# Optimization experiments

Hardware: AMD Instinct MI355X
Metric: run time of the kernel (lower is better)

The kernel has to match this reference:

```python
import jax, jax.numpy as jnp
import numpy as np

B, S, D, H, DH = 2, 1024, 1024, 16, 64
SCALE = 1.0 / np.sqrt(DH)


def setup_inputs() -> dict:
    key = jax.random.key(0)
    ks = jax.random.split(key, 9)
    return {
        "x": jax.random.normal(ks[0], (B, S, D), jnp.float32),
        "qkv_w": jax.random.normal(ks[1], (3 * H * DH, D), jnp.float32) * 0.02,
        "out_w": jax.random.normal(ks[2], (D, H * DH), jnp.float32) * 0.02,
        "bias_p": jax.random.uniform(ks[3], (H, 1, 1), jnp.float32) * 2.0,
        "bias_a": jax.random.uniform(ks[4], (H, 1, 1), jnp.float32),
        "mlp_w1": jax.random.normal(ks[5], (H, 2 * H), jnp.float32) * 0.1,
        "mlp_b1": jnp.zeros((H,), jnp.float32),
        "mlp_w2": jax.random.normal(ks[6], (H, H), jnp.float32) * 0.1,
        "mlp_b2": jnp.zeros((H,), jnp.float32),
    }


def reference(x, qkv_w, out_w, bias_p, bias_a, mlp_w1, mlp_b1, mlp_w2, mlp_b2):
    # qkv projection: torch Linear => x @ W.T
    qkv = (x @ qkv_w.T).reshape(B, S, 3, H, DH)
    q = qkv[:, :, 0].transpose(0, 2, 1, 3)  # [B,H,S,DH]
    k = qkv[:, :, 1].transpose(0, 2, 1, 3)
    v = qkv[:, :, 2].transpose(0, 2, 1, 3)

    scores = jnp.einsum('bhqd,bhkd->bhqk', q, k) * SCALE  # [B,H,S,S]

    # Kerple additive bias: -p * log1p(a * |i-j|), per head
    p = jnp.clip(bias_p, 0.01)
    a = jnp.clip(bias_a, 0.01)
    pos = jnp.arange(S, dtype=jnp.float32)
    dist = jnp.abs(pos[None, :] - pos[:, None])  # [S,S]
    kb = -p * jnp.log1p(a * dist)  # [H,S,S]

    # DAPE refinement MLP over per-(i,j) head features
    z = jnp.concatenate(
        [scores, jnp.broadcast_to(kb[None], (B, H, S, S))], axis=1
    ).transpose(0, 2, 3, 1)  # [B,S,S,2H]
    hdn = jax.nn.gelu(z @ mlp_w1.T + mlp_b1, approximate=False)  # [B,S,S,H]
    refine = (hdn @ mlp_w2.T + mlp_b2).transpose(0, 3, 1, 2)  # [B,H,S,S]

    scores = scores + kb[None] + refine
    attn = jax.nn.softmax(scores, axis=-1)  # dropout is identity in eval

    out = jnp.einsum('bhqk,bhkd->bhqd', attn, v)  # [B,H,S,DH]
    out = out.transpose(0, 2, 1, 3).reshape(B, S, H * DH)
    return out @ out_w.T
```

## Files before the change

### kernel.cpp

```cpp
#include <hip/hip_runtime.h>
#include <math.h>

#define Bsz 2
#define Ssz 1024
#define Dsz 1024
#define Hn 16
#define DHsz 64
#define QKV3 3072
#define SCALE 0.125f

typedef __bf16 bf16;
typedef bf16 bf16x8 __attribute__((ext_vector_type(8)));
typedef bf16 bf16x4 __attribute__((ext_vector_type(4)));
typedef float f32x4 __attribute__((ext_vector_type(4)));

#define MFMA(a, b, c) __builtin_amdgcn_mfma_f32_16x16x32_bf16(a, b, c, 0, 0, 0)
#define LDT 72

__global__ void cast_hi(const float* __restrict__ src, bf16* __restrict__ hi, int n) {
  int idx = (blockIdx.x * 256 + threadIdx.x) * 4;
  if (idx >= n) return;
  float4 v = *(const float4*)(src + idx);
  bf16x4 hv = {(bf16)v.x, (bf16)v.y, (bf16)v.z, (bf16)v.w};
  *(bf16x4*)(hi + idx) = hv;
}

__global__ void kb_table(const float* __restrict__ bias_p, const float* __restrict__ bias_a,
                         float* __restrict__ kbtt) {
  int idx = blockIdx.x * 256 + threadIdx.x;
  int d = idx >> 4, h = idx & 15;
  float p = fmaxf(bias_p[h], 0.01f), a = fmaxf(bias_a[h], 0.01f);
  kbtt[idx] = -p * log1pf(a * (float)d);
}

__global__ void tk_table(const float* __restrict__ kbtt, const float* __restrict__ w1,
                         const float* __restrict__ b1, float2* __restrict__ tk) {
  int idx = blockIdx.x * 256 + threadIdx.x;
  int o = idx >> 4, n = idx & 15;
  int d = o - 1024; if (d < 0) d = -d; if (d > 1023) d = 1023;
  float t1 = b1[n];
#pragma unroll
  for (int h = 0; h < 16; ++h) t1 += w1[n * 32 + 16 + h] * kbtt[d * 16 + h];
  tk[idx] = make_float2(t1, kbtt[d * 16 + n]);
}

__global__ void wfrag(const float* __restrict__ w1, const float* __restrict__ w2,
                      bf16* __restrict__ wf) {
  int lane = threadIdx.x;
  int l15 = lane & 15, q8 = (lane >> 4) << 3;
  bf16x8 w1d, w2a;
#pragma unroll
  for (int e = 0; e < 8; ++e) {
    int k = q8 + e;
    if (k < 16) {
      w1d[e] = (bf16)w1[l15 * 32 + k];
    } else {
      float w = w1[l15 * 32 + k - 16];
      w1d[e] = (bf16)(w - (float)(bf16)w);
    }
    w2a[e] = (bf16)w2[l15 * 16 + (k & 15)];
  }
  *(bf16x8*)(wf + lane * 8) = w1d;
  *(bf16x8*)(wf + 512 + lane * 8) = w2a;
}

__global__ __launch_bounds__(256, 3) void k1_qkv(const bf16* __restrict__ A,
                                                 const bf16* __restrict__ B,
                                                 bf16* __restrict__ C) {
  __shared__ __align__(16) bf16 sA[128 * LDT];
  __shared__ __align__(16) bf16 sB[96 * LDT];
  const int tid = threadIdx.x;
  const int lane = tid & 63, wv = tid >> 6;
  const int wr = wv >> 1, wc = wv & 1;
  const int l15 = lane & 15, q8 = (lane >> 4) << 3, q4 = (lane >> 4) << 2;
  const int m0 = blockIdx.y * 128, n0 = blockIdx.x * 96;
  const int r0 = tid >> 3, c8 = (tid & 7) << 3;

  f32x4 acc[4][3];
#pragma unroll
  for (int t = 0; t < 4; ++t)
#pragma unroll
    for (int u = 0; u < 3; ++u)
#pragma unroll
      for (int r = 0; r < 4; ++r) acc[t][u][r] = 0.f;

  bf16x8 rA[4], rB[3];
#define K1_LOAD(kt)                                                         \
  {                                                                         \
    _Pragma("unroll") for (int c = 0; c < 4; ++c)                           \
      rA[c] = *(const bf16x8*)(A + (size_t)(m0 + c * 32 + r0) * Dsz + (kt) + c8);  \
    _Pragma("unroll") for (int c = 0; c < 3; ++c)                           \
      rB[c] = *(const bf16x8*)(B + (size_t)(n0 + c * 32 + r0) * Dsz + (kt) + c8);  \
  }

  K1_LOAD(0)
  for (int kt = 0; kt < Dsz; kt += 64) {
    __syncthreads();
#pragma unroll
    for (int c = 0; c < 4; ++c) *(bf16x8*)&sA[(c * 32 + r0) * LDT + c8] = rA[c];
#pragma unroll
    for (int c = 0; c < 3; ++c) *(bf16x8*)&sB[(c * 32 + r0) * LDT + c8] = rB[c];
    __syncthreads();
    if (kt + 64 < Dsz) K1_LOAD(kt + 64)
#pragma unroll
    for (int ks = 0; ks < 64; ks += 32) {
      bf16x8 fa[4], fb[3];
#pragma unroll
      for (int t = 0; t < 4; ++t)
        fa[t] = *(const bf16x8*)&sA[(wr * 64 + t * 16 + l15) * LDT + ks + q8];
#pragma unroll
      for (int u = 0; u < 3; ++u)
        fb[u] = *(const bf16x8*)&sB[(wc * 48 + u * 16 + l15) * LDT + ks + q8];
#pragma unroll
      for (int t = 0; t < 4; ++t)
#pragma unroll
        for (int u = 0; u < 3; ++u) acc[t][u] = MFMA(fa[t], fb[u], acc[t][u]);
    }
  }
#pragma unroll
  for (int t = 0; t < 4; ++t)
#pragma unroll
    for (int u = 0; u < 3; ++u) {
      int col = n0 + wc * 48 + u * 16 + l15;
#pragma unroll
      for (int r = 0; r < 4; ++r) {
        int row = m0 + wr * 64 + t * 16 + q4 + r;
        C[(size_t)row * QKV3 + col] = (bf16)acc[t][u][r];
      }
    }
#undef K1_LOAD
}

__global__ void pack_vt(const bf16* __restrict__ qkv, bf16* __restrict__ vt) {
  __shared__ __align__(16) bf16 T[64 * LDT];
  const int tid = threadIdx.x;
  const int bh = blockIdx.y, b = bh >> 4, h = bh & 15;
  const int j0 = blockIdx.x * 64;
#pragma unroll
  for (int c = 0; c < 2; ++c) {
    int lin = c * 256 + tid;
    int jr = lin >> 3, d8 = (lin & 7) << 3;
    bf16x8 v = *(const bf16x8*)(qkv + (size_t)(b * Ssz + j0 + jr) * QKV3 + 2048 + h * DHsz + d8);
#pragma unroll
    for (int e = 0; e < 8; ++e) T[(d8 + e) * LDT + jr] = v[e];
  }
  __syncthreads();
#pragma unroll
  for (int c = 0; c < 2; ++c) {
    int lin = c * 256 + tid;
    int d = lin >> 3, j8 = (lin & 7) << 3;
    bf16x8 o = *(const bf16x8*)&T[d * LDT + j8];
    *(bf16x8*)(vt + ((size_t)(b * Hn + h) * DHsz + d) * Ssz + j0 + j8) = o;
  }
}

__global__ __launch_bounds__(256, 3) void k2_qk(const bf16* __restrict__ qkv,
                                                bf16* __restrict__ scores) {
  __shared__ __align__(16) bf16 sA[128 * LDT], sB[128 * LDT];
  const int tid = threadIdx.x;
  const int lane = tid & 63, wv = tid >> 6;
  const int wr = wv >> 1, wc = wv & 1;
  const int l15 = lane & 15, q8 = (lane >> 4) << 3, q4 = (lane >> 4) << 2;
  const int z = blockIdx.z, b = z >> 4, h = z & 15;
  const int i0 = blockIdx.y * 128, j0 = blockIdx.x * 128;
  const bf16* Ab = qkv + (size_t)b * Ssz * QKV3 + h * DHsz;
  const bf16* Bb = Ab + Ssz;
  const int r0 = tid >> 3, c8 = (tid & 7) << 3;
#pragma unroll
  for (int c = 0; c < 4; ++c) {
    int row = c * 32 + r0;
    *(bf16x8*)&sA[row * LDT + c8] = *(const bf16x8*)(Ab + (size_t)(i0 + row) * QKV3 + c8);
    *(bf16x8*)&sB[row * LDT + c8] = *(const bf16x8*)(Bb + (size_t)(j0 + row) * QKV3 + c8);
  }
  __syncthreads();
  f32x4 acc[4][4];
#pragma unroll
  for (int t = 0; t < 4; ++t)
#pragma unroll
    for (int u = 0; u < 4; ++u)
#pragma unroll
      for (int r = 0; r < 4; ++r) acc[t][u][r] = 0.f;
#pragma unroll
  for (int ks = 0; ks < 64; ks += 32) {
    bf16x8 fa[4], fb[4];
#pragma unroll
    for (int t = 0; t < 4; ++t) fa[t] = *(const bf16x8*)&sA[(wr * 64 + t * 16 + l15) * LDT + ks + q8];
#pragma unroll
    for (int u = 0; u < 4; ++u) fb[u] = *(const bf16x8*)&sB[(wc * 64 + u * 16 + l15) * LDT + ks + q8];
#pragma unroll
    for (int t = 0; t < 4; ++t)
#pragma unroll
      for (int u = 0; u < 4; ++u) acc[t][u] = MFMA(fa[t], fb[u], acc[t][u]);
  }
  bf16* dstp = scores + ((size_t)(b * Hn + h) << 20);
#pragma unroll
  for (int t = 0; t < 4; ++t)
#pragma unroll
    for (int u = 0; u < 4; ++u) {
      int col = j0 + wc * 64 + u * 16 + l15;
#pragma unroll
      for (int r = 0; r < 4; ++r) {
        int row = i0 + wr * 64 + t * 16 + q4 + r;
        dstp[((size_t)row << 10) + col] = (bf16)(acc[t][u][r] * SCALE);
      }
    }
}

__device__ __forceinline__ float gelu_fast(float x) {
  float z = fabsf(x) * 0.70710678118654752f;
  float t = __builtin_amdgcn_rcpf(fmaf(0.3275911f, z, 1.0f));
  float poly = t * fmaf(t, fmaf(t, fmaf(t, fmaf(t, 1.061405429f, -1.453152027f),
                                        1.421413741f), -0.284496736f), 0.254829592f);
  float erfa = 1.0f - poly * __expf(-z * z);
  float erfs = copysignf(erfa, x);
  return 0.5f * x * (1.0f + erfs);
}

#define SHS 264
#define LGS 264

__global__ __launch_bounds__(256, 5) void dape_softmax(bf16* scores,
                                                       const float2* __restrict__ tk,
                                                       const bf16* __restrict__ wf,
                                                       const float* __restrict__ b2,
                                                       float* __restrict__ sums) {
  const int c = blockIdx.x;
  const int i = blockIdx.y;
  const int b = blockIdx.z;
  const int tid = threadIdx.x;
  const int lane = tid & 63, wv = tid >> 6;
  const int l15 = lane & 15, q = lane >> 4;
  const int q8 = q << 3, q4 = q << 2;

  __shared__ bf16 sH[Hn][SHS];
  __shared__ float lgt[Hn][LGS];
  __shared__ __align__(16) bf16 hdnS[4][16][40];

  const bf16x8 w1d = *(const bf16x8*)(wf + lane * 8);
  const bf16x8 w2a = *(const bf16x8*)(wf + 512 + lane * 8);
  const float bias2 = b2[l15];

  if (lane < 32) {
    int row = lane >> 1, col = 16 + (lane & 1) * 8;
    *(bf16x8*)&hdnS[wv][row][col] = (bf16x8){};
  }

  const int jw = wv * 64;
  const bf16* srow = scores + ((size_t)(b * Hn) << 20) + ((size_t)i << 10) + c * 256;
#pragma unroll
  for (int t = 0; t < 2; ++t) {
    int h = t * 8 + (lane >> 3);
    int col = jw + (lane & 7) * 8;
    *(bf16x8*)&sH[h][col] = *(const bf16x8*)(srow + ((size_t)h << 20) + col);
  }

  const float2* tkp = tk + ((size_t)(c * 256 + jw + q4 - i + 1024) << 4) + l15;

  for (int jt = 0; jt < 4; ++jt) {
    const int j0c = jw + jt * 16;
    bf16x8 a1;
#pragma unroll
    for (int e = 0; e < 8; ++e) a1[e] = sH[(q8 + e) & 15][j0c + l15];
    float2 tkv[4];
#pragma unroll
    for (int r = 0; r < 4; ++r) tkv[r] = tkp[r * 16];
    f32x4 c1 = {tkv[0].x, tkv[1].x, tkv[2].x, tkv[3].x};
    c1 = MFMA(a1, w1d, c1);
#pragma unroll
    for (int r = 0; r < 4; ++r) hdnS[wv][q4 + r][l15] = (bf16)gelu_fast(c1[r]);
    bf16x8 a2 = *(const bf16x8*)&hdnS[wv][l15][q8];
    f32x4 c2 = {bias2, bias2, bias2, bias2};
    c2 = MFMA(a2, w2a, c2);
    bf16x4 sc4 = *(const bf16x4*)&sH[l15][j0c + q4];
    f32x4 lg;
#pragma unroll
    for (int r = 0; r < 4; ++r) lg[r] = (float)sc4[r] + tkv[r].y + c2[r];
    *(f32x4*)&lgt[l15][j0c + q4] = lg;
    tkp += 256;
  }
  __syncthreads();

#pragma unroll
  for (int hh = 0; hh < 4; ++hh) {
    const int h = wv * 4 + hh;
    f32x4 v0 = *(const f32x4*)&lgt[h][lane * 4];
    float s = 0.f;
#pragma unroll
    for (int e = 0; e < 4; ++e) { v0[e] = __expf(v0[e]); s += v0[e]; }
#pragma unroll
    for (int off = 32; off > 0; off >>= 1) s += __shfl_xor(s, off, 64);
    bf16* dst = scores + ((size_t)(b * Hn + h) << 20) + ((size_t)i << 10) + c * 256;
    bf16x4 p0 = {(bf16)v0[0], (bf16)v0[1], (bf16)v0[2], (bf16)v0[3]};
    *(bf16x4*)(dst + lane * 4) = p0;
    if (lane == 0) sums[((((b << 10) + i) << 4) + h) * 4 + c] = s;
  }
}

__global__ __launch_bounds__(256, 4) void k4_av(const bf16* __restrict__ attn,
                                                const bf16* __restrict__ vt,
                                                const float* __restrict__ sums,
                                                bf16* __restrict__ aout) {
  __shared__ __align__(16) bf16 sA[64 * LDT], sB[64 * LDT];
  const int tid = threadIdx.x;
  const int lane = tid & 63, wv = tid >> 6;
  const int wr = wv >> 1, wc = wv & 1;
  const int l15 = lane & 15, q8 = (lane >> 4) << 3, q4 = (lane >> 4) << 2;
  const int i0 = blockIdx.x * 64, h = blockIdx.y, b = blockIdx.z;
  const bf16* Ab = attn + ((size_t)(b * Hn + h) << 20) + ((size_t)i0 << 10);
  const bf16* Bb = vt + (size_t)(b * Hn + h) * DHsz * Ssz;
  const int r0 = tid >> 3, c8 = (tid & 7) << 3;
  f32x4 acc[2][2];
#pragma unroll
  for (int t = 0; t < 2; ++t)
#pragma unroll
    for (int u = 0; u < 2; ++u)
#pragma unroll
      for (int r = 0; r < 4; ++r) acc[t][u][r] = 0.f;
  bf16x8 rA[2], rB[2];
#define K4_LOAD(kt)                                               \
  {                                                               \
    _Pragma("unroll") for (int c = 0; c < 2; ++c) {               \
      int row = c * 32 + r0;                                      \
      rA[c] = *(const bf16x8*)(Ab + ((size_t)row << 10) + (kt) + c8); \
      rB[c] = *(const bf16x8*)(Bb + ((size_t)row << 10) + (kt) + c8); \
    }                                                             \
  }
  K4_LOAD(0)
  for (int kt = 0; kt < Ssz; kt += 64) {
    __syncthreads();
#pragma unroll
    for (int c = 0; c < 2; ++c) {
      int row = c * 32 + r0;
      *(bf16x8*)&sA[row * LDT + c8] = rA[c];
      *(bf16x8*)&sB[row * LDT + c8] = rB[c];
    }
    __syncthreads();
    if (kt + 64 < Ssz) K4_LOAD(kt + 64)
#pragma unroll
    for (int ks = 0; ks < 64; ks += 32) {
      bf16x8 fa[2], fb[2];
#pragma unroll
      for (int t = 0; t < 2; ++t) fa[t] = *(const bf16x8*)&sA[(wr * 32 + t * 16 + l15) * LDT + ks + q8];
#pragma unroll
      for (int u = 0; u < 2; ++u) fb[u] = *(const bf16x8*)&sB[(wc * 32 + u * 16 + l15) * LDT + ks + q8];
#pragma unroll
      for (int t = 0; t < 2; ++t)
#pragma unroll
        for (int u = 0; u < 2; ++u) acc[t][u] = MFMA(fa[t], fb[u], acc[t][u]);
    }
  }
#pragma unroll
  for (int t = 0; t < 2; ++t)
#pragma unroll
    for (int r = 0; r < 4; ++r) {
      int row = i0 + wr * 32 + t * 16 + q4 + r;
      f32x4 sv = *(const f32x4*)&sums[((((b << 10) + row) << 4) + h) * 4];
      float inv = 1.f / (sv[0] + sv[1] + sv[2] + sv[3]);
#pragma unroll
      for (int u = 0; u < 2; ++u) {
        int d = wc * 32 + u * 16 + l15;
        aout[(size_t)(b * Ssz + row) * Dsz + h * DHsz + d] = (bf16)(acc[t][u][r] * inv);
      }
    }
#undef K4_LOAD
}

__global__ __launch_bounds__(256, 4) void k5_out(const bf16* __restrict__ A,
                                                 const bf16* __restrict__ B,
                                                 float* __restrict__ C) {
  __shared__ __align__(16) bf16 sA[64 * LDT], sB[64 * LDT];
  const int tid = threadIdx.x;
  const int lane = tid & 63, wv = tid >> 6;
  const int wr = wv >> 1, wc = wv & 1;
  const int l15 = lane & 15, q8 = (lane >> 4) << 3, q4 = (lane >> 4) << 2;
  const int m0 = blockIdx.y * 64, n0 = blockIdx.x * 64;
  const int r0 = tid >> 3, c8 = (tid & 7) << 3;
  f32x4 acc[2][2];
#pragma unroll
  for (int t = 0; t < 2; ++t)
#pragma unroll
    for (int u = 0; u < 2; ++u)
#pragma unroll
      for (int r = 0; r < 4; ++r) acc[t][u][r] = 0.f;
  bf16x8 rA[2], rB[2];
#define K5_LOAD(kt)                                                       \
  {                                                                       \
    _Pragma("unroll") for (int c = 0; c < 2; ++c) {                       \
      int row = c * 32 + r0;                                              \
      rA[c] = *(const bf16x8*)(A + (size_t)(m0 + row) * Dsz + (kt) + c8);   \
      rB[c] = *(const bf16x8*)(B + (size_t)(n0 + row) * Dsz + (kt) + c8);   \
    }                                                                     \
  }
  K5_LOAD(0)
  for (int kt = 0; kt < Dsz; kt += 64) {
    __syncthreads();
#pragma unroll
    for (int c = 0; c < 2; ++c) {
      int row = c * 32 + r0;
      *(bf16x8*)&sA[row * LDT + c8] = rA[c];
      *(bf16x8*)&sB[row * LDT + c8] = rB[c];
    }
    __syncthreads();
    if (kt + 64 < Dsz) K5_LOAD(kt + 64)
#pragma unroll
    for (int ks = 0; ks < 64; ks += 32) {
      bf16x8 fa[2], fb[2];
#pragma unroll
      for (int t = 0; t < 2; ++t) fa[t] = *(const bf16x8*)&sA[(wr * 32 + t * 16 + l15) * LDT + ks + q8];
#pragma unroll
      for (int u = 0; u < 2; ++u) fb[u] = *(const bf16x8*)&sB[(wc * 32 + u * 16 + l15) * LDT + ks + q8];
#pragma unroll
      for (int t = 0; t < 2; ++t)
#pragma unroll
        for (int u = 0; u < 2; ++u) acc[t][u] = MFMA(fa[t], fb[u], acc[t][u]);
    }
  }
#pragma unroll
  for (int t = 0; t < 2; ++t)
#pragma unroll
    for (int u = 0; u < 2; ++u) {
      int col = n0 + wc * 32 + u * 16 + l15;
#pragma unroll
      for (int r = 0; r < 4; ++r) {
        int row = m0 + wr * 32 + t * 16 + q4 + r;
        C[(size_t)row * Dsz + col] = acc[t][u][r];
      }
    }
#undef K5_LOAD
}

extern "C" void kernel_launch(void* const* d_in, const int* in_sizes, int n_in,
                              void* d_out, int out_size, void* d_ws, size_t ws_size,
                              hipStream_t stream) {
  const float* x      = (const float*)d_in[0];
  const float* qkv_w  = (const float*)d_in[1];
  const float* out_w  = (const float*)d_in[2];
  const float* bias_p = (const float*)d_in[3];
  const float* bias_a = (const float*)d_in[4];
  const float* w1     = (const float*)d_in[5];
  const float* b1     = (const float*)d_in[6];
  const float* w2     = (const float*)d_in[7];
  const float* b2     = (const float*)d_in[8];
  float* out = (float*)d_out;

  char* ws = (char*)d_ws;
  const size_t MB = 1ull << 20;
  bf16* ow_h   = (bf16*)(ws + 0 * MB);
  bf16* qkv_bf = (bf16*)(ws + 2 * MB);
  bf16* v_t    = (bf16*)(ws + 14 * MB);
  bf16* aout   = (bf16*)(ws + 18 * MB);
  float* kbtt  = (float*)(ws + 22 * MB);
  float* sums  = (float*)(ws + 22 * MB + 65536);
  bf16* wf     = (bf16*)(ws + 22 * MB + 589824);
  float2* tk   = (float2*)(ws + 22 * MB + 655360);
  bf16* x_h    = (bf16*)(ws + 23 * MB);
  bf16* w_h    = (bf16*)(ws + 27 * MB);
  bf16* sc_bf  = (bf16*)(ws + 23 * MB);

  cast_hi<<<2048, 256, 0, stream>>>(x, x_h, Bsz * Ssz * Dsz);
  cast_hi<<<3072, 256, 0, stream>>>(qkv_w, w_h, QKV3 * Dsz);
  cast_hi<<<1024, 256, 0, stream>>>(out_w, ow_h, Dsz * Dsz);
  kb_table<<<64, 256, 0, stream>>>(bias_p, bias_a, kbtt);
  tk_table<<<128, 256, 0, stream>>>(kbtt, w1, b1, tk);
  wfrag<<<1, 64, 0, stream>>>(w1, w2, wf);

  k1_qkv<<<dim3(QKV3 / 96, (Bsz * Ssz) / 128), 256, 0, stream>>>(x_h, w_h, qkv_bf);
  pack_vt<<<dim3(Ssz / 64, Bsz * Hn), 256, 0, stream>>>(qkv_bf, v_t);

  k2_qk<<<dim3(Ssz / 128, Ssz / 128, Bsz * Hn), 256, 0, stream>>>(qkv_bf, sc_bf);
  dape_softmax<<<dim3(4, Ssz, Bsz), 256, 0, stream>>>(sc_bf, tk, wf, b2, sums);
  k4_av<<<dim3(Ssz / 64, Hn, Bsz), 256, 0, stream>>>(sc_bf, v_t, sums, aout);

  k5_out<<<dim3(Dsz / 64, (Bsz * Ssz) / 64), 256, 0, stream>>>(aout, ow_h, out);
}
```

Baseline: 205.7 us.

## Fuse setup kernels and compute softmax exponentials in the DAPE MFMA loop

```diff
diff --git a/kernel.cpp b/kernel.cpp
--- a/kernel.cpp
+++ b/kernel.cpp
@@ -17,51 +17,63 @@
 #define MFMA(a, b, c) __builtin_amdgcn_mfma_f32_16x16x32_bf16(a, b, c, 0, 0, 0)
 #define LDT 72
 
-__global__ void cast_hi(const float* __restrict__ src, bf16* __restrict__ hi, int n) {
+__global__ void cast_all(const float* __restrict__ x, const float* __restrict__ qw,
+                         const float* __restrict__ ow, bf16* __restrict__ xh,
+                         bf16* __restrict__ wh, bf16* __restrict__ owh) {
   int idx = (blockIdx.x * 256 + threadIdx.x) * 4;
-  if (idx >= n) return;
-  float4 v = *(const float4*)(src + idx);
+  const float* src;
+  bf16* dst;
+  int off = idx;
+  if (idx < 2097152) {
+    src = x; dst = xh;
+  } else if (idx < 2097152 + 3145728) {
+    src = qw; dst = wh; off = idx - 2097152;
+  } else {
+    src = ow; dst = owh; off = idx - (2097152 + 3145728);
+  }
+  float4 v = *(const float4*)(src + off);
   bf16x4 hv = {(bf16)v.x, (bf16)v.y, (bf16)v.z, (bf16)v.w};
-  *(bf16x4*)(hi + idx) = hv;
-}
-
-__global__ void kb_table(const float* __restrict__ bias_p, const float* __restrict__ bias_a,
-                         float* __restrict__ kbtt) {
-  int idx = blockIdx.x * 256 + threadIdx.x;
-  int d = idx >> 4, h = idx & 15;
-  float p = fmaxf(bias_p[h], 0.01f), a = fmaxf(bias_a[h], 0.01f);
-  kbtt[idx] = -p * log1pf(a * (float)d);
-}
-
-__global__ void tk_table(const float* __restrict__ kbtt, const float* __restrict__ w1,
-                         const float* __restrict__ b1, float2* __restrict__ tk) {
+  *(bf16x4*)(dst + off) = hv;
+}
+
+__global__ void tk_wfrag(const float* __restrict__ bias_p, const float* __restrict__ bias_a,
+                         const float* __restrict__ w1, const float* __restrict__ b1,
+                         const float* __restrict__ w2, float2* __restrict__ tk,
+                         bf16* __restrict__ wf) {
+  if (blockIdx.x == 128) {
+    int lane = threadIdx.x;
+    if (lane < 64) {
+      int l15 = lane & 15, q8 = (lane >> 4) << 3;
+      bf16x8 w1d, w2a;
+#pragma unroll
+      for (int e = 0; e < 8; ++e) {
+        int k = q8 + e;
+        if (k < 16) {
+          w1d[e] = (bf16)w1[l15 * 32 + k];
+        } else {
+          float w = w1[l15 * 32 + k - 16];
+          w1d[e] = (bf16)(w - (float)(bf16)w);
+        }
+        w2a[e] = (bf16)w2[l15 * 16 + (k & 15)];
+      }
+      *(bf16x8*)(wf + lane * 8) = w1d;
+      *(bf16x8*)(wf + 512 + lane * 8) = w2a;
+    }
+    return;
+  }
   int idx = blockIdx.x * 256 + threadIdx.x;
   int o = idx >> 4, n = idx & 15;
   int d = o - 1024; if (d < 0) d = -d; if (d > 1023) d = 1023;
+  float fd = (float)d;
   float t1 = b1[n];
-#pragma unroll
-  for (int h = 0; h < 16; ++h) t1 += w1[n * 32 + 16 + h] * kbtt[d * 16 + h];
-  tk[idx] = make_float2(t1, kbtt[d * 16 + n]);
-}
-
-__global__ void wfrag(const float* __restrict__ w1, const float* __restrict__ w2,
-                      bf16* __restrict__ wf) {
-  int lane = threadIdx.x;
-  int l15 = lane & 15, q8 = (lane >> 4) << 3;
-  bf16x8 w1d, w2a;
-#pragma unroll
-  for (int e = 0; e < 8; ++e) {
-    int k = q8 + e;
-    if (k < 16) {
-      w1d[e] = (bf16)w1[l15 * 32 + k];
-    } else {
-      float w = w1[l15 * 32 + k - 16];
-      w1d[e] = (bf16)(w - (float)(bf16)w);
-    }
-    w2a[e] = (bf16)w2[l15 * 16 + (k & 15)];
-  }
-  *(bf16x8*)(wf + lane * 8) = w1d;
-  *(bf16x8*)(wf + 512 + lane * 8) = w2a;
+  float t2 = 0.f;
+#pragma unroll
+  for (int h = 0; h < 16; ++h) {
+    float kb = -fmaxf(bias_p[h], 0.01f) * log1pf(fmaxf(bias_a[h], 0.01f) * fd);
+    t1 += w1[n * 32 + 16 + h] * kb;
+    if (h == n) t2 = kb;
+  }
+  tk[idx] = make_float2(t1, t2);
 }
 
 __global__ __launch_bounds__(256, 3) void k1_qkv(const bf16* __restrict__ A,
@@ -217,9 +229,8 @@
 }
 
 #define SHS 264
-#define LGS 264
-
-__global__ __launch_bounds__(256, 5) void dape_softmax(bf16* scores,
+
+__global__ __launch_bounds__(256, 6) void dape_softmax(bf16* scores,
                                                        const float2* __restrict__ tk,
                                                        const bf16* __restrict__ wf,
                                                        const float* __restrict__ b2,
@@ -233,8 +244,8 @@
   const int q8 = q << 3, q4 = q << 2;
 
   __shared__ bf16 sH[Hn][SHS];
-  __shared__ float lgt[Hn][LGS];
   __shared__ __align__(16) bf16 hdnS[4][16][40];
+  __shared__ float sumLDS[4][16];
 
   const bf16x8 w1d = *(const bf16x8*)(wf + lane * 8);
   const bf16x8 w2a = *(const bf16x8*)(wf + 512 + lane * 8);
@@ -246,7 +257,7 @@
   }
 
   const int jw = wv * 64;
-  const bf16* srow = scores + ((size_t)(b * Hn) << 20) + ((size_t)i << 10) + c * 256;
+  bf16* srow = scores + ((size_t)(b * Hn) << 20) + ((size_t)i << 10) + c * 256;
 #pragma unroll
   for (int t = 0; t < 2; ++t) {
     int h = t * 8 + (lane >> 3);
@@ -255,6 +266,8 @@
   }
 
   const float2* tkp = tk + ((size_t)(c * 256 + jw + q4 - i + 1024) << 4) + l15;
+  bf16* prow = srow + ((size_t)l15 << 20) + jw;
+  float psum = 0.f;
 
   for (int jt = 0; jt < 4; ++jt) {
     const int j0c = jw + jt * 16;
@@ -272,27 +285,25 @@
     f32x4 c2 = {bias2, bias2, bias2, bias2};
     c2 = MFMA(a2, w2a, c2);
     bf16x4 sc4 = *(const bf16x4*)&sH[l15][j0c + q4];
-    f32x4 lg;
-#pragma unroll
-    for (int r = 0; r < 4; ++r) lg[r] = (float)sc4[r] + tkv[r].y + c2[r];
-    *(f32x4*)&lgt[l15][j0c + q4] = lg;
+    f32x4 pv;
+#pragma unroll
+    for (int r = 0; r < 4; ++r) {
+      float lg = (float)sc4[r] + tkv[r].y + c2[r];
+      pv[r] = __expf(lg);
+      psum += pv[r];
+    }
+    bf16x4 p4 = {(bf16)pv[0], (bf16)pv[1], (bf16)pv[2], (bf16)pv[3]};
+    *(bf16x4*)(prow + jt * 16 + q4) = p4;
     tkp += 256;
   }
+
+  psum += __shfl_xor(psum, 16, 64);
+  psum += __shfl_xor(psum, 32, 64);
+  if (lane < 16) sumLDS[wv][lane] = psum;
   __syncthreads();
-
-#pragma unroll
-  for (int hh = 0; hh < 4; ++hh) {
-    const int h = wv * 4 + hh;
-    f32x4 v0 = *(const f32x4*)&lgt[h][lane * 4];
-    float s = 0.f;
-#pragma unroll
-    for (int e = 0; e < 4; ++e) { v0[e] = __expf(v0[e]); s += v0[e]; }
-#pragma unroll
-    for (int off = 32; off > 0; off >>= 1) s += __shfl_xor(s, off, 64);
-    bf16* dst = scores + ((size_t)(b * Hn + h) << 20) + ((size_t)i << 10) + c * 256;
-    bf16x4 p0 = {(bf16)v0[0], (bf16)v0[1], (bf16)v0[2], (bf16)v0[3]};
-    *(bf16x4*)(dst + lane * 4) = p0;
-    if (lane == 0) sums[((((b << 10) + i) << 4) + h) * 4 + c] = s;
+  if (tid < 16) {
+    float tot = sumLDS[0][tid] + sumLDS[1][tid] + sumLDS[2][tid] + sumLDS[3][tid];
+    sums[((((b << 10) + i) << 4) + tid) * 4 + c] = tot;
   }
 }
 
@@ -449,7 +460,6 @@
   bf16* qkv_bf = (bf16*)(ws + 2 * MB);
   bf16* v_t    = (bf16*)(ws + 14 * MB);
   bf16* aout   = (bf16*)(ws + 18 * MB);
-  float* kbtt  = (float*)(ws + 22 * MB);
   float* sums  = (float*)(ws + 22 * MB + 65536);
   bf16* wf     = (bf16*)(ws + 22 * MB + 589824);
   float2* tk   = (float2*)(ws + 22 * MB + 655360);
@@ -457,12 +467,8 @@
   bf16* w_h    = (bf16*)(ws + 27 * MB);
   bf16* sc_bf  = (bf16*)(ws + 23 * MB);
 
-  cast_hi<<<2048, 256, 0, stream>>>(x, x_h, Bsz * Ssz * Dsz);
-  cast_hi<<<3072, 256, 0, stream>>>(qkv_w, w_h, QKV3 * Dsz);
-  cast_hi<<<1024, 256, 0, stream>>>(out_w, ow_h, Dsz * Dsz);
-  kb_table<<<64, 256, 0, stream>>>(bias_p, bias_a, kbtt);
-  tk_table<<<128, 256, 0, stream>>>(kbtt, w1, b1, tk);
-  wfrag<<<1, 64, 0, stream>>>(w1, w2, wf);
+  cast_all<<<6144, 256, 0, stream>>>(x, qkv_w, out_w, x_h, w_h, ow_h);
+  tk_wfrag<<<129, 256, 0, stream>>>(bias_p, bias_a, w1, b1, w2, tk, wf);
 
   k1_qkv<<<dim3(QKV3 / 96, (Bsz * Ssz) / 128), 256, 0, stream>>>(x_h, w_h, qkv_bf);
   pack_vt<<<dim3(Ssz / 64, Bsz * Hn), 256, 0, stream>>>(qkv_bf, v_t);
```

New measurement: 204.6 us. No clear change (-0.6%).
